# Kernel optimization log

Hardware: AMD Instinct MI355X
Metric: run time of the kernel (lower is better)

The kernel has to match this reference:

```python
import jax, jax.numpy as jnp
import numpy as np

B, R, C_M, C_Z, H, DH, NQP = 2, 384, 384, 128, 12, 32, 4
W_C = (2.0 / (9 * NQP)) ** (-0.5)   # (2/(9*n_qp))^-0.5
W_L = 3.0 ** 0.5                     # (1/3)^-0.5


def setup_inputs() -> dict:
    key = jax.random.key(0)
    ks = jax.random.split(key, 10)
    pair_rep = jax.random.normal(ks[0], (B, R, R, C_Z), jnp.float32)
    sing_rep = jax.random.normal(ks[1], (B, R, C_M), jnp.float32)
    m = jax.random.normal(ks[2], (B, R, 3, 3), jnp.float32)
    bbr, _ = jnp.linalg.qr(m)  # orthonormal backbone frames (B,R,3,3)
    bbt = jax.random.normal(ks[3], (B, R, 3), jnp.float32)
    s = 0.02
    W_qkv = jax.random.normal(ks[4], (C_M, DH * 3 * H), jnp.float32) * s
    W_qk = jax.random.normal(ks[5], (C_M, H * 2 * NQP * 3), jnp.float32) * s
    W_fc1 = jax.random.normal(ks[6], (C_Z, H), jnp.float32) * s
    b_fc1 = jnp.zeros((H,), jnp.float32)
    W0 = jax.random.normal(ks[7], (H * DH, C_M), jnp.float32) * s
    W1 = jax.random.normal(ks[8], (H * C_Z, C_M), jnp.float32) * s
    gamma = jax.random.uniform(ks[9], (1,), jnp.float32)
    return dict(pair_rep=pair_rep, sing_rep=sing_rep, bbr=bbr, bbt=bbt,
                W_qkv=W_qkv, W_qk=W_qk, W_fc1=W_fc1, b_fc1=b_fc1,
                W0=W0, W1=W1, gamma=gamma)


def reference(pair_rep, sing_rep, bbr, bbt, W_qkv, W_qk, W_fc1, b_fc1, W0, W1, gamma):
    # pair bias: fc1 then b i j h -> b h i j
    pair_bias = jnp.transpose(jnp.einsum('bijc,ch->bijh', pair_rep, W_fc1) + b_fc1,
                              (0, 3, 1, 2))                      # b h i j
    # scalar q/k/v: channel layout (dim_head, 3, heads)
    qkv = (sing_rep @ W_qkv).reshape(B, R, DH, 3, H)
    rq, rk, rv = (jnp.transpose(qkv[:, :, :, i, :], (0, 3, 1, 2)) for i in range(3))  # b h r d
    dot = jnp.einsum('bhid,bhjd->bhij', rq, rk) * DH ** (-0.5)
    # point q/k: channel layout (heads, 2, n_qp, 3)
    qk = (sing_rep @ W_qk).reshape(B, R, H, 2, NQP, 3)
    gq = jnp.transpose(qk[:, :, :, 0], (0, 3, 1, 2, 4))          # b p r h a
    gk = jnp.transpose(qk[:, :, :, 1], (0, 3, 1, 2, 4))
    # frame-transformed query/key points
    Tq = jnp.einsum('bprha,brak->phbrk', gq, bbr) + bbt          # p h b r 3
    Tk = jnp.einsum('bprha,brak->phbrk', gk, bbr) + bbt
    diff = Tq[:, :, :, :, None, :] - Tk[:, :, :, None, :, :]     # p h b i j 3
    sq = jnp.transpose(jnp.sum(diff * diff, axis=(0, -1)), (1, 0, 2, 3))  # b h i j
    head_w = jax.nn.softplus(gamma[0]) * W_C / 2                 # same scalar per head
    attn = jax.nn.softmax(W_L * (pair_bias + dot + head_w * sq), axis=-1)
    # pair-rep value aggregation -> W_1
    top = jnp.einsum('bhij,bijc->bihc', attn, pair_rep).reshape(B, R, H * C_Z) @ W1
    # scalar value aggregation -> W_0   (note: original adds these two only;
    # the point-value 'bot' branch is computed but unused in the output)
    out = jnp.transpose(jnp.einsum('bhij,bhjd->bhid', attn, rv),
                        (0, 2, 1, 3)).reshape(B, R, H * DH) @ W0
    return out + top
```

## Files before the change

kernel.cpp:

```cpp
#include <hip/hip_runtime.h>
#include <math.h>

#define Bb   2
#define Rr   384
#define CMd  384
#define CZ   128
#define Hh   12
#define DHd  32

#define WL           1.7320508075688772f
#define WC           4.242640687119285f
#define INV_SQRT_DH  0.17677669529663687f

#define SZ_R   (Bb*Hh*Rr*DHd)
#define SZ_T   (Bb*Hh*Rr*12)
#define SZ_S   (Bb*Hh*Rr)
#define SZ_A   ((long)Bb*Hh*Rr*Rr)
#define SZ_O   (Bb*Rr*Hh*DHd)

#define G_BM 64
#define G_BN 64
#define G_BK 32
__global__ __launch_bounds__(256) void k_projgemm(
    const float* __restrict__ sing, const float* __restrict__ Wqkv,
    const float* __restrict__ Wqk,
    float* __restrict__ rq, float* __restrict__ rk, float* __restrict__ rv,
    float* __restrict__ gbuf)
{
  const int t = threadIdx.x;
  const int m0 = blockIdx.x * G_BM;
  const int n0 = blockIdx.y * G_BN;
  const int tx = t & 15, ty = t >> 4;
  __shared__ float As[G_BK][G_BM + 4];
  __shared__ float Bs[G_BK][G_BN + 4];
  float acc[4][4] = {};

  for (int kc = 0; kc < 384; kc += G_BK) {
    for (int l = t; l < 512; l += 256) {
      int row = l >> 3;
      int k4  = (l & 7) << 2;
      float4 v = *(const float4*)(sing + (long)(m0 + row)*384 + kc + k4);
      As[k4  ][row] = v.x; As[k4+1][row] = v.y;
      As[k4+2][row] = v.z; As[k4+3][row] = v.w;
    }
    for (int l = t; l < 512; l += 256) {
      int k  = l >> 4;
      int c4 = (l & 15) << 2;
      int n  = n0 + c4;
      int gk = kc + k;
      float4 v;
      if (n < 1152)      v = *(const float4*)(Wqkv + (long)gk*1152 + n);
      else if (n < 1440) v = *(const float4*)(Wqk  + (long)gk*288 + (n - 1152));
      else               v = make_float4(0.f, 0.f, 0.f, 0.f);
      Bs[k][c4] = v.x; Bs[k][c4+1] = v.y; Bs[k][c4+2] = v.z; Bs[k][c4+3] = v.w;
    }
    __syncthreads();
    #pragma unroll
    for (int k = 0; k < G_BK; ++k) {
      float4 a = *(const float4*)&As[k][ty*4];
      float4 b = *(const float4*)&Bs[k][tx*4];
      acc[0][0] += a.x*b.x; acc[0][1] += a.x*b.y; acc[0][2] += a.x*b.z; acc[0][3] += a.x*b.w;
      acc[1][0] += a.y*b.x; acc[1][1] += a.y*b.y; acc[1][2] += a.y*b.z; acc[1][3] += a.y*b.w;
      acc[2][0] += a.z*b.x; acc[2][1] += a.z*b.y; acc[2][2] += a.z*b.z; acc[2][3] += a.z*b.w;
      acc[3][0] += a.w*b.x; acc[3][1] += a.w*b.y; acc[3][2] += a.w*b.z; acc[3][3] += a.w*b.w;
    }
    __syncthreads();
  }
  #pragma unroll
  for (int j = 0; j < 4; ++j) {
    int n = n0 + tx*4 + j;
    if (n >= 1440) continue;
    if (n < 1152) {
      int d = n/36, rem = n - d*36, which = rem/12, h = rem - which*12;
      float* dst = (which == 0) ? rq : (which == 1) ? rk : rv;
      #pragma unroll
      for (int i = 0; i < 4; ++i) {
        int row = m0 + ty*4 + i, b = row / Rr, r = row - b*Rr;
        dst[(((long)b*Hh + h)*Rr + r)*DHd + d] = acc[i][j];
      }
    } else {
      int c2 = n - 1152;
      #pragma unroll
      for (int i = 0; i < 4; ++i)
        gbuf[(long)(m0 + ty*4 + i)*288 + c2] = acc[i][j];
    }
  }
}

__global__ __launch_bounds__(256) void k_frame(
    const float* __restrict__ gbuf, const float* __restrict__ bbr,
    const float* __restrict__ bbt,
    float* __restrict__ TqF, float* __restrict__ TkF,
    float* __restrict__ Qsq, float* __restrict__ Ksq)
{
  const int idx = blockIdx.x*256 + threadIdx.x;
  const int row = idx / 24, q = idx - row*24;
  const int h = q >> 1, s2 = q & 1;
  const float* gp = gbuf + (long)row*288 + h*24 + s2*12;
  float rot[9], tr[3];
  #pragma unroll
  for (int a = 0; a < 9; ++a) rot[a] = bbr[(long)row*9 + a];
  #pragma unroll
  for (int a = 0; a < 3; ++a) tr[a] = bbt[(long)row*3 + a];
  const int b = row / Rr, r = row - b*Rr;
  float* T = s2 ? TkF : TqF;
  const long tb = (((long)b*Hh + h)*Rr + r)*12;
  float v[12]; float ss = 0.f;
  #pragma unroll
  for (int p = 0; p < 4; ++p)
    #pragma unroll
    for (int k2 = 0; k2 < 3; ++k2) {
      float x = gp[p*3+0]*rot[k2] + gp[p*3+1]*rot[3+k2] + gp[p*3+2]*rot[6+k2] + tr[k2];
      v[p*3+k2] = x; ss += x*x;
    }
  *(float4*)(T + tb)     = make_float4(v[0], v[1], v[2],  v[3]);
  *(float4*)(T + tb + 4) = make_float4(v[4], v[5], v[6],  v[7]);
  *(float4*)(T + tb + 8) = make_float4(v[8], v[9], v[10], v[11]);
  (s2 ? Ksq : Qsq)[((long)b*Hh + h)*Rr + r] = ss;
}

__global__ __launch_bounds__(256) void k_pbias(
    const float* __restrict__ pair, const float* __restrict__ Wfc1,
    const float* __restrict__ bfc1, float* __restrict__ pb)
{
  const int t = threadIdx.x;
  const long base = (long)blockIdx.x * 64;
  __shared__ float tile[64][129];
  __shared__ float w_l[128][12];
  __shared__ float bias_l[12];
  for (int idx = t; idx < 128*12; idx += 256) w_l[idx/12][idx%12] = Wfc1[idx];
  if (t < 12) bias_l[t] = bfc1[t];
  const float4* src = (const float4*)(pair + base*CZ);
  for (int idx = t; idx < 64*32; idx += 256) {
    float4 v = src[idx];
    int row = idx >> 5, c4 = (idx & 31) << 2;
    tile[row][c4] = v.x; tile[row][c4+1] = v.y; tile[row][c4+2] = v.z; tile[row][c4+3] = v.w;
  }
  __syncthreads();
  int row = t & 63;
  long n = base + row;
  int b = (int)(n / ((long)Rr*Rr));
  long rr2 = n - (long)b*Rr*Rr;
  int i = (int)(rr2 / Rr), j = (int)(rr2 - (long)i*Rr);
  int h0 = t >> 6;
  float a0 = bias_l[h0], a1 = bias_l[h0+4], a2 = bias_l[h0+8];
  for (int c = 0; c < 128; ++c) {
    float v = tile[row][c];
    a0 += v*w_l[c][h0]; a1 += v*w_l[c][h0+4]; a2 += v*w_l[c][h0+8];
  }
  long o = (((long)b*Hh + h0)*Rr + i)*Rr + j;
  const long hstride = (long)Rr*Rr*4;
  pb[o] = a0; pb[o + hstride] = a1; pb[o + 2*hstride] = a2;
}

#define ITILE 8
__global__ __launch_bounds__(256) void k_scores(
    const float* __restrict__ rq, const float* __restrict__ rk,
    const float* __restrict__ TqF, const float* __restrict__ TkF,
    const float* __restrict__ Qsq, const float* __restrict__ Ksq,
    const float* __restrict__ gamma, float* __restrict__ attn)
{
  const int t = threadIdx.x;
  const int nt = Rr / ITILE;
  const int bh = blockIdx.x / nt;
  const int i0 = (blockIdx.x - bh*nt) * ITILE;
  __shared__ float rk_l[384][33];
  __shared__ float rq_l[32];
  __shared__ float tq_l[12];
  __shared__ float scal[1];
  __shared__ float redm[4], reds[4];

  for (int idx = t; idx < 384*32; idx += 256)
    rk_l[idx >> 5][idx & 31] = rk[(long)bh*Rr*DHd + idx];

  const float g0 = gamma[0];
  const float head_w = log1pf(__expf(g0)) * (WC * 0.5f);

  for (int ii = 0; ii < ITILE; ++ii) {
    const int i = i0 + ii;
    if (t < 32) rq_l[t] = rq[((long)bh*Rr + i)*DHd + t];
    if (t < 12) tq_l[t] = TqF[((long)bh*Rr + i)*12 + t];
    if (t == 0) scal[0] = Qsq[(long)bh*Rr + i];
    __syncthreads();
    const float qs = scal[0];
    const long rowbase = ((long)bh*Rr + i)*Rr;

    auto logit_at = [&](int j) -> float {
      float dt = 0.f;
      #pragma unroll
      for (int dd = 0; dd < 32; ++dd) dt += rq_l[dd] * rk_l[j][dd];
      const float4* tk = (const float4*)(TkF + ((long)bh*Rr + j)*12);
      float4 ta = tk[0], tb = tk[1], tc = tk[2];
      float pt = tq_l[0]*ta.x + tq_l[1]*ta.y + tq_l[2]*ta.z + tq_l[3]*ta.w
               + tq_l[4]*tb.x + tq_l[5]*tb.y + tq_l[6]*tb.z + tq_l[7]*tb.w
               + tq_l[8]*tc.x + tq_l[9]*tc.y + tq_l[10]*tc.z + tq_l[11]*tc.w;
      float sqv = qs + Ksq[(long)bh*Rr + j] - 2.f*pt;
      return WL * (attn[rowbase + j] + dt*INV_SQRT_DH + head_w*sqv);
    };

    float l0 = logit_at(t);
    float l1 = (t < 128) ? logit_at(t + 256) : -3.4e38f;
    float m = fmaxf(l0, l1);
    #pragma unroll
    for (int s = 32; s; s >>= 1) m = fmaxf(m, __shfl_xor(m, s, 64));
    if ((t & 63) == 0) redm[t >> 6] = m;
    __syncthreads();
    m = fmaxf(fmaxf(redm[0], redm[1]), fmaxf(redm[2], redm[3]));
    float e0 = __expf(l0 - m);
    float e1 = (t < 128) ? __expf(l1 - m) : 0.f;
    float s = e0 + e1;
    #pragma unroll
    for (int sh = 32; sh; sh >>= 1) s += __shfl_xor(s, sh, 64);
    if ((t & 63) == 0) reds[t >> 6] = s;
    __syncthreads();
    float inv = 1.f / (reds[0] + reds[1] + reds[2] + reds[3]);
    attn[rowbase + t] = e0 * inv;
    if (t < 128) attn[rowbase + t + 256] = e1 * inv;
    __syncthreads();
  }
}

__global__ __launch_bounds__(256) void k_agg(
    const float* __restrict__ attn, const float* __restrict__ pair,
    const float* __restrict__ rv, float* __restrict__ o_ihd, float* __restrict__ top)
{
  const int t = threadIdx.x;
  const int bi = blockIdx.x;
  const int by = blockIdx.y;
  const int b = bi / Rr;
  const int i = bi - b*Rr;
  __shared__ float a_l[12][384];
  for (int idx = t; idx < 12*384; idx += 256) {
    int h = idx / 384, j = idx - h*384;
    a_l[h][j] = attn[(((long)b*Hh + h)*Rr + i)*Rr + j];
  }
  __syncthreads();
  const int c = (t & 63) + (by << 6);
  const int hg = t >> 6;
  const float* prow = pair + (long)bi * Rr * CZ;
  float acc0 = 0.f, acc1 = 0.f, acc2 = 0.f;
  #pragma unroll 4
  for (int j = 0; j < 384; ++j) {
    float v = prow[(long)j*CZ + c];
    acc0 += a_l[hg  ][j]*v;
    acc1 += a_l[hg+4][j]*v;
    acc2 += a_l[hg+8][j]*v;
  }
  float* tp = top + ((long)bi*Hh)*CZ + c;
  tp[(long)(hg  )*CZ] = acc0;
  tp[(long)(hg+4)*CZ] = acc1;
  tp[(long)(hg+8)*CZ] = acc2;
  if (t < 192) {
    const int o = by*192 + t;
    int h = o >> 5, dd = o & 31;
    const float* rvp = rv + ((long)b*Hh + h)*Rr*DHd + dd;
    float s = 0.f;
    #pragma unroll 4
    for (int j = 0; j < 384; ++j) s += a_l[h][j] * rvp[(long)j*DHd];
    o_ihd[(long)bi*384 + o] = s;
  }
}

#define K5_KSPLIT 6
#define K5_KLEN   320
__global__ __launch_bounds__(256) void k_final_part(
    const float* __restrict__ o_ihd, const float* __restrict__ top,
    const float* __restrict__ W0, const float* __restrict__ W1,
    float* __restrict__ partial)
{
  const int t = threadIdx.x;
  const int m0 = blockIdx.x * 64;
  const int n0 = blockIdx.y * 64;
  const int ks = blockIdx.z;
  const int tx = t & 15, ty = t >> 4;
  __shared__ float As[32][68];
  __shared__ float Bs[32][68];
  float acc[4][4] = {};

  const int kbeg = ks * K5_KLEN;
  for (int kc = kbeg; kc < kbeg + K5_KLEN; kc += 32) {
    for (int l = t; l < 512; l += 256) {
      int row = l >> 3;
      int k4  = (l & 7) << 2;
      int gk  = kc + k4;
      const float* src;
      if (gk < 384) src = o_ihd + (long)(m0 + row)*384 + gk;
      else          src = top   + (long)(m0 + row)*1536 + (gk - 384);
      float4 v = *(const float4*)src;
      As[k4  ][row] = v.x; As[k4+1][row] = v.y;
      As[k4+2][row] = v.z; As[k4+3][row] = v.w;
    }
    for (int l = t; l < 512; l += 256) {
      int k  = l >> 4;
      int c4 = (l & 15) << 2;
      int gk = kc + k;
      const float* src;
      if (gk < 384) src = W0 + (long)gk*384 + n0 + c4;
      else          src = W1 + (long)(gk - 384)*384 + n0 + c4;
      float4 v = *(const float4*)src;
      Bs[k][c4] = v.x; Bs[k][c4+1] = v.y; Bs[k][c4+2] = v.z; Bs[k][c4+3] = v.w;
    }
    __syncthreads();
    #pragma unroll
    for (int k = 0; k < 32; ++k) {
      float4 a = *(const float4*)&As[k][ty*4];
      float4 b = *(const float4*)&Bs[k][tx*4];
      acc[0][0] += a.x*b.x; acc[0][1] += a.x*b.y; acc[0][2] += a.x*b.z; acc[0][3] += a.x*b.w;
      acc[1][0] += a.y*b.x; acc[1][1] += a.y*b.y; acc[1][2] += a.y*b.z; acc[1][3] += a.y*b.w;
      acc[2][0] += a.z*b.x; acc[2][1] += a.z*b.y; acc[2][2] += a.z*b.z; acc[2][3] += a.z*b.w;
      acc[3][0] += a.w*b.x; acc[3][1] += a.w*b.y; acc[3][2] += a.w*b.z; acc[3][3] += a.w*b.w;
    }
    __syncthreads();
  }
  float* pdst = partial + (long)ks * (768*384);
  #pragma unroll
  for (int i = 0; i < 4; ++i) {
    int row = m0 + ty*4 + i;
    #pragma unroll
    for (int j = 0; j < 4; ++j)
      pdst[(long)row*384 + n0 + tx*4 + j] = acc[i][j];
  }
}

__global__ __launch_bounds__(256) void k_final_reduce(
    const float* __restrict__ partial, float* __restrict__ out)
{
  const int idx = blockIdx.x*256 + threadIdx.x;
  float4 r = make_float4(0.f, 0.f, 0.f, 0.f);
  #pragma unroll
  for (int p = 0; p < K5_KSPLIT; ++p) {
    float4 a = ((const float4*)(partial + (long)p*768*384))[idx];
    r.x += a.x; r.y += a.y; r.z += a.z; r.w += a.w;
  }
  ((float4*)out)[idx] = r;
}

extern "C" void kernel_launch(void* const* d_in, const int* in_sizes, int n_in,
                              void* d_out, int out_size, void* d_ws, size_t ws_size,
                              hipStream_t stream)
{
  (void)in_sizes; (void)n_in; (void)out_size; (void)ws_size;
  const float* pair  = (const float*)d_in[0];
  const float* sing  = (const float*)d_in[1];
  const float* bbr   = (const float*)d_in[2];
  const float* bbt   = (const float*)d_in[3];
  const float* Wqkv  = (const float*)d_in[4];
  const float* Wqk   = (const float*)d_in[5];
  const float* Wfc1  = (const float*)d_in[6];
  const float* bfc1  = (const float*)d_in[7];
  const float* W0    = (const float*)d_in[8];
  const float* W1    = (const float*)d_in[9];
  const float* gamma = (const float*)d_in[10];
  float* out = (float*)d_out;

  float* ws    = (float*)d_ws;
  float* rq    = ws;
  float* rk    = rq  + SZ_R;
  float* rv    = rk  + SZ_R;
  float* TqF   = rv  + SZ_R;
  float* TkF   = TqF + SZ_T;
  float* Qsq   = TkF + SZ_T;
  float* Ksq   = Qsq + SZ_S;
  float* attn  = Ksq + SZ_S;
  float* o_ihd = attn + SZ_A;
  float* top   = o_ihd + SZ_O;
  float* gbuf  = o_ihd;
  float* partial = attn;

  k_projgemm<<<dim3(Bb*Rr/G_BM, (1440 + G_BN - 1)/G_BN), dim3(256), 0, stream>>>(
      sing, Wqkv, Wqk, rq, rk, rv, gbuf);
  k_frame<<<dim3(Bb*Rr*24/256), dim3(256), 0, stream>>>(
      gbuf, bbr, bbt, TqF, TkF, Qsq, Ksq);
  k_pbias<<<dim3(Bb*Rr*Rr/64), dim3(256), 0, stream>>>(pair, Wfc1, bfc1, attn);
  k_scores<<<dim3(Bb*Hh*(Rr/ITILE)), dim3(256), 0, stream>>>(
      rq, rk, TqF, TkF, Qsq, Ksq, gamma, attn);
  k_agg<<<dim3(Bb*Rr, 2), dim3(256), 0, stream>>>(attn, pair, rv, o_ihd, top);
  k_final_part<<<dim3(Bb*Rr/64, 384/64, K5_KSPLIT), dim3(256), 0, stream>>>(
      o_ihd, top, W0, W1, partial);
  k_final_reduce<<<dim3(768*384/4/256), dim3(256), 0, stream>>>(partial, out);
}
```

Measured before the change: 235.9 us.

## Restructure score softmax to one wave per row and drop per-row constant

```diff
diff --git a/kernel.cpp b/kernel.cpp
--- a/kernel.cpp
+++ b/kernel.cpp
@@ -153,70 +153,79 @@
   pb[o] = a0; pb[o + hstride] = a1; pb[o + 2*hstride] = a2;
 }
 
-#define ITILE 8
+#define ITILE 16
 __global__ __launch_bounds__(256) void k_scores(
     const float* __restrict__ rq, const float* __restrict__ rk,
     const float* __restrict__ TqF, const float* __restrict__ TkF,
-    const float* __restrict__ Qsq, const float* __restrict__ Ksq,
-    const float* __restrict__ gamma, float* __restrict__ attn)
+    const float* __restrict__ Ksq, const float* __restrict__ gamma,
+    float* __restrict__ attn)
 {
   const int t = threadIdx.x;
   const int nt = Rr / ITILE;
   const int bh = blockIdx.x / nt;
   const int i0 = (blockIdx.x - bh*nt) * ITILE;
+  const int w  = t >> 6;
+  const int lane = t & 63;
   __shared__ float rk_l[384][33];
-  __shared__ float rq_l[32];
-  __shared__ float tq_l[12];
-  __shared__ float scal[1];
-  __shared__ float redm[4], reds[4];
+  __shared__ float tk_l[384][13];
+  __shared__ float ksq_l[384];
 
   for (int idx = t; idx < 384*32; idx += 256)
     rk_l[idx >> 5][idx & 31] = rk[(long)bh*Rr*DHd + idx];
+  for (int idx = t; idx < 384*12; idx += 256)
+    tk_l[idx / 12][idx % 12] = TkF[(long)bh*Rr*12 + idx];
+  for (int idx = t; idx < 384; idx += 256)
+    ksq_l[idx] = Ksq[(long)bh*Rr + idx];
 
   const float g0 = gamma[0];
   const float head_w = log1pf(__expf(g0)) * (WC * 0.5f);
-
-  for (int ii = 0; ii < ITILE; ++ii) {
-    const int i = i0 + ii;
-    if (t < 32) rq_l[t] = rq[((long)bh*Rr + i)*DHd + t];
-    if (t < 12) tq_l[t] = TqF[((long)bh*Rr + i)*12 + t];
-    if (t == 0) scal[0] = Qsq[(long)bh*Rr + i];
-    __syncthreads();
-    const float qs = scal[0];
+  __syncthreads();
+
+  for (int ii = 0; ii < 4; ++ii) {
+    const int i = i0 + w*4 + ii;
     const long rowbase = ((long)bh*Rr + i)*Rr;
-
-    auto logit_at = [&](int j) -> float {
+    float rq_v[32], tq_v[12];
+    {
+      const float4* qp = (const float4*)(rq + ((long)bh*Rr + i)*DHd);
+      #pragma unroll
+      for (int q4 = 0; q4 < 8; ++q4) {
+        float4 v = qp[q4];
+        rq_v[q4*4] = v.x; rq_v[q4*4+1] = v.y; rq_v[q4*4+2] = v.z; rq_v[q4*4+3] = v.w;
+      }
+      const float4* tp = (const float4*)(TqF + ((long)bh*Rr + i)*12);
+      #pragma unroll
+      for (int q4 = 0; q4 < 3; ++q4) {
+        float4 v = tp[q4];
+        tq_v[q4*4] = v.x; tq_v[q4*4+1] = v.y; tq_v[q4*4+2] = v.z; tq_v[q4*4+3] = v.w;
+      }
+    }
+    float lg[6];
+    #pragma unroll
+    for (int jj = 0; jj < 6; ++jj) {
+      const int j = lane + jj*64;
       float dt = 0.f;
       #pragma unroll
-      for (int dd = 0; dd < 32; ++dd) dt += rq_l[dd] * rk_l[j][dd];
-      const float4* tk = (const float4*)(TkF + ((long)bh*Rr + j)*12);
-      float4 ta = tk[0], tb = tk[1], tc = tk[2];
-      float pt = tq_l[0]*ta.x + tq_l[1]*ta.y + tq_l[2]*ta.z + tq_l[3]*ta.w
-               + tq_l[4]*tb.x + tq_l[5]*tb.y + tq_l[6]*tb.z + tq_l[7]*tb.w
-               + tq_l[8]*tc.x + tq_l[9]*tc.y + tq_l[10]*tc.z + tq_l[11]*tc.w;
-      float sqv = qs + Ksq[(long)bh*Rr + j] - 2.f*pt;
-      return WL * (attn[rowbase + j] + dt*INV_SQRT_DH + head_w*sqv);
-    };
-
-    float l0 = logit_at(t);
-    float l1 = (t < 128) ? logit_at(t + 256) : -3.4e38f;
-    float m = fmaxf(l0, l1);
+      for (int dd = 0; dd < 32; ++dd) dt += rq_v[dd] * rk_l[j][dd];
+      float pt = 0.f;
+      #pragma unroll
+      for (int cc = 0; cc < 12; ++cc) pt += tq_v[cc] * tk_l[j][cc];
+      float pbv = attn[rowbase + j];
+      lg[jj] = WL * (pbv + dt*INV_SQRT_DH + head_w*(ksq_l[j] - 2.f*pt));
+    }
+    float m = lg[0];
+    #pragma unroll
+    for (int jj = 1; jj < 6; ++jj) m = fmaxf(m, lg[jj]);
     #pragma unroll
     for (int s = 32; s; s >>= 1) m = fmaxf(m, __shfl_xor(m, s, 64));
-    if ((t & 63) == 0) redm[t >> 6] = m;
-    __syncthreads();
-    m = fmaxf(fmaxf(redm[0], redm[1]), fmaxf(redm[2], redm[3]));
-    float e0 = __expf(l0 - m);
-    float e1 = (t < 128) ? __expf(l1 - m) : 0.f;
-    float s = e0 + e1;
-    #pragma unroll
-    for (int sh = 32; sh; sh >>= 1) s += __shfl_xor(s, sh, 64);
-    if ((t & 63) == 0) reds[t >> 6] = s;
-    __syncthreads();
-    float inv = 1.f / (reds[0] + reds[1] + reds[2] + reds[3]);
-    attn[rowbase + t] = e0 * inv;
-    if (t < 128) attn[rowbase + t + 256] = e1 * inv;
-    __syncthreads();
+    float e[6]; float sum = 0.f;
+    #pragma unroll
+    for (int jj = 0; jj < 6; ++jj) { e[jj] = __expf(lg[jj] - m); sum += e[jj]; }
+    #pragma unroll
+    for (int s = 32; s; s >>= 1) sum += __shfl_xor(sum, s, 64);
+    const float inv = 1.f / sum;
+    #pragma unroll
+    for (int jj = 0; jj < 6; ++jj)
+      attn[rowbase + lane + jj*64] = e[jj] * inv;
   }
 }
 
@@ -261,8 +270,8 @@
   }
 }
 
-#define K5_KSPLIT 6
-#define K5_KLEN   320
+#define K5_KSPLIT 4
+#define K5_KLEN   480
 __global__ __launch_bounds__(256) void k_final_part(
     const float* __restrict__ o_ihd, const float* __restrict__ top,
     const float* __restrict__ W0, const float* __restrict__ W1,
@@ -373,7 +382,7 @@
       gbuf, bbr, bbt, TqF, TkF, Qsq, Ksq);
   k_pbias<<<dim3(Bb*Rr*Rr/64), dim3(256), 0, stream>>>(pair, Wfc1, bfc1, attn);
   k_scores<<<dim3(Bb*Hh*(Rr/ITILE)), dim3(256), 0, stream>>>(
-      rq, rk, TqF, TkF, Qsq, Ksq, gamma, attn);
+      rq, rk, TqF, TkF, Ksq, gamma, attn);
   k_agg<<<dim3(Bb*Rr, 2), dim3(256), 0, stream>>>(attn, pair, rv, o_ihd, top);
   k_final_part<<<dim3(Bb*Rr/64, 384/64, K5_KSPLIT), dim3(256), 0, stream>>>(
       o_ihd, top, W0, W1, partial);
```

Result: slower. 247.1 us (+4.8%).
